# Optimization experiments

Measured on AMD Instinct MI355X. Metric: run time of the kernel, lower is better.

Reference implementation:

```python
import jax, jax.numpy as jnp
import numpy as np

H, DH = 8, 64            # heads, dim_head (inner_dim = 512)
W_DOT = 1.0              # mask_cond['para']['w_dot']
TOTAL_STEP = 50


def split_heads(x):
    # 'b n (h d) -> (b h) n d'
    b, n, _ = x.shape
    return x.reshape(b, n, H, DH).transpose(0, 2, 1, 3).reshape(b * H, n, DH)


def merge_heads(x):
    # '(b h) n d -> b n (h d)'
    bh, n, d = x.shape
    b = bh // H
    return x.reshape(b, H, n, d).transpose(0, 2, 1, 3).reshape(b, n, H * d)


def setup_inputs() -> dict:
    key = jax.random.key(0)
    ks = jax.random.split(key, 10)
    B, N, DQ, DC, L, C = 1, 4096, 320, 768, 77, 4
    INNER = H * DH
    w = lambda i, shape: jax.random.normal(ks[i], shape, jnp.float32) * 0.02
    return {
        "x": jax.random.normal(ks[0], (2 * B, N, DQ), jnp.float32),
        "uc_context": jax.random.normal(ks[1], (B, L, DC), jnp.float32),
        "ck": jax.random.normal(ks[2], (C, B, L, DC), jnp.float32),
        "cv": jax.random.normal(ks[3], (C, B, L, DC), jnp.float32),
        "attn_extra": jax.random.uniform(ks[4], (H, N, L), jnp.float32),
        "Wq": w(5, (DQ, INNER)),
        "Wk": w(6, (DC, INNER)),
        "Wv": w(7, (DC, INNER)),
        "Wo": w(8, (INNER, DQ)),
        "bo": jnp.zeros((DQ,), jnp.float32),
        "t": 10,
    }


def reference(x, uc_context, ck, cv, attn_extra, Wq, Wk, Wv, Wo, bo, t):
    scale = DH ** (-0.5)
    # schedule()['linear'][TOTAL_STEP - t - 1] == t / 50 * 4.6
    weight = (t / TOTAL_STEP) * 4.6

    B = uc_context.shape[0]
    true_bs = B * H

    q = split_heads(x @ Wq)                          # [(2B)H, N, d]
    k_uc = split_heads(uc_context @ Wk)              # [BH, L, d]
    v_uc = split_heads(uc_context @ Wv)
    k_c = jax.vmap(lambda c: split_heads(c @ Wk))(ck)  # [C, BH, L, d]
    v_c = jax.vmap(lambda c: split_heads(c @ Wv))(cv)

    q_uc, q_c = q[:true_bs], q[true_bs:]
    sim_uc = jnp.einsum('bid,bjd->bij', q_uc, k_uc) * scale     # [BH, N, L]
    sim_c = jnp.einsum('bid,cbjd->cbij', q_c, k_c) * scale      # [C, BH, N, L]

    # region-dependent additive soft mask on the first conditional branch,
    # weighted by w_dot * schedule_weight * max(sim_c[0])
    wmask = W_DOT * weight * sim_c[0].max()
    sim_c = sim_c.at[0].add(wmask * attn_extra)     # attn_extra [H, N, L] broadcasts (B=1)

    attn_uc = jax.nn.softmax(sim_uc, axis=-1)
    attn_c = jax.nn.softmax(sim_c, axis=-1)

    out_uc = jnp.einsum('bij,bjd->bid', attn_uc, v_uc)
    out_c = jnp.einsum('cbij,cbjd->bid', attn_c, v_c) / v_c.shape[0]

    out = jnp.concatenate([out_uc, out_c], axis=0)  # [2BH, N, d]
    out = merge_heads(out)                          # [2B, N, inner]
    return out @ Wo + bo                            # to_out (dropout=0 -> identity)
```

## Files before the change

### kernel.cpp

```cpp
#include <hip/hip_runtime.h>


typedef __attribute__((ext_vector_type(8))) short          bf16x8;
typedef __attribute__((ext_vector_type(4))) float          f32x4;
typedef __attribute__((ext_vector_type(8))) unsigned short u16x8;

#define OFF_XB    0ull
#define OFF_CTXB  5242880ull
#define OFF_WQT   6307328ull
#define OFF_WKT   6635008ull
#define OFF_WVT   7421440ull
#define OFF_WOT   8207872ull
#define OFF_QB    8535552ull
#define OFF_KB    16924160ull
#define OFF_VTB   17333760ull
#define OFF_ATT0  18152960ull
#define OFF_ATTC  22347264ull
#define OFF_MAX   39124480ull

#define SMEM_BYTES 38400

struct Params {
  const float *x, *uc, *ck, *cv, *ex, *Wq, *Wk, *Wv, *Wo, *bo;
  const int* tp;
  unsigned short *xb, *ctxb, *WqT, *WkT, *WvT, *WoT, *qb, *kb, *vtb, *att0, *attc;
  unsigned* maxslot;
  float* out;
};

__device__ __forceinline__ unsigned short bf_cvt(float f) {
  unsigned u = __float_as_uint(f);
  unsigned r = u + 0x7FFFu + ((u >> 16) & 1u);
  return (unsigned short)(r >> 16);
}
__device__ __forceinline__ float bf2f(unsigned short u) {
  return __uint_as_float(((unsigned)u) << 16);
}
__device__ __forceinline__ unsigned enc_f(float f) {
  int b = __float_as_int(f);
  return (b >= 0) ? ((unsigned)b | 0x80000000u) : ~(unsigned)b;
}
__device__ __forceinline__ float dec_f(unsigned u) {
  unsigned b = (u & 0x80000000u) ? (u ^ 0x80000000u) : ~u;
  return __int_as_float((int)b);
}
__device__ __forceinline__ f32x4 mfma16(bf16x8 a, bf16x8 b, f32x4 c) {
  return __builtin_amdgcn_mfma_f32_16x16x32_bf16(a, b, c, 0, 0, 0);
}
__device__ __forceinline__ void gload16(const void* g, void* l) {
  __builtin_amdgcn_global_load_lds((const __attribute__((address_space(1))) void*)g,
                                   (__attribute__((address_space(3))) void*)l, 16, 0, 0);
}

__global__ void __launch_bounds__(256, 4) k_all(Params p, int ph) {
  __shared__ __align__(16) char smem[SMEM_BYTES];
  const int tid  = threadIdx.x;
  const int lane = tid & 63, w = tid >> 6;
  const int l15  = lane & 15, qd = lane >> 4;
  const int v = blockIdx.x;

  if (ph == 0) {
    if (v < 2560) {
      size_t idx = (size_t)v * 256 + tid;
      float4 t = reinterpret_cast<const float4*>(p.x)[idx];
      ushort4 o = {bf_cvt(t.x), bf_cvt(t.y), bf_cvt(t.z), bf_cvt(t.w)};
      reinterpret_cast<ushort4*>(p.xb)[idx] = o;
      if (v == 0 && tid == 0) *p.maxslot = 0u;
    } else if (v < 3080) {
      size_t r = (size_t)(v - 2560) * 256 + tid;
      if (r < 133056) {
        const float4* s = (r < 14784) ? (reinterpret_cast<const float4*>(p.uc) + r)
                        : (r < 73920) ? (reinterpret_cast<const float4*>(p.ck) + (r - 14784))
                                      : (reinterpret_cast<const float4*>(p.cv) + (r - 73920));
        float4 t = *s;
        ushort4 o = {bf_cvt(t.x), bf_cvt(t.y), bf_cvt(t.z), bf_cvt(t.w)};
        reinterpret_cast<ushort4*>(p.ctxb)[r] = o;
      }
    } else {
      int q = v - 3080;
      const float* src; unsigned short* dst; int R, C, rt, ct;
      if (q < 160)      { src = p.Wq; dst = p.WqT; R = 320; C = 512; rt = q / 16; ct = q % 16; }
      else if (q < 544) { q -= 160; src = p.Wk; dst = p.WkT; R = 768; C = 512; rt = q / 16; ct = q % 16; }
      else if (q < 928) { q -= 544; src = p.Wv; dst = p.WvT; R = 768; C = 512; rt = q / 16; ct = q % 16; }
      else              { q -= 928; src = p.Wo; dst = p.WoT; R = 512; C = 320; rt = q / 10; ct = q % 10; }
      float* T = reinterpret_cast<float*>(smem);
      int r0 = rt * 32, c0 = ct * 32;
      { int r = tid >> 3, c4 = (tid & 7) * 4;
        float4 t = *reinterpret_cast<const float4*>(src + (size_t)(r0 + r) * C + c0 + c4);
        T[r * 33 + c4] = t.x; T[r * 33 + c4 + 1] = t.y;
        T[r * 33 + c4 + 2] = t.z; T[r * 33 + c4 + 3] = t.w; }
      __syncthreads();
      { int c = tid >> 3, r4 = (tid & 7) * 4;
        ushort4 o = {bf_cvt(T[r4 * 33 + c]), bf_cvt(T[(r4 + 1) * 33 + c]),
                     bf_cvt(T[(r4 + 2) * 33 + c]), bf_cvt(T[(r4 + 3) * 33 + c])};
        *reinterpret_cast<ushort4*>(dst + (size_t)(c0 + c) * R + r0 + r4) = o; }
    }
  }

  else if (ph == 1) {
    if (v < 512) {
      int mb = (v >> 3) * 128, nb = (v & 7) * 64;
      unsigned short* As = reinterpret_cast<unsigned short*>(smem);
      unsigned short* Bs = reinterpret_cast<unsigned short*>(smem + 8192);
      int wr = w >> 1, wc = w & 1;
      f32x4 acc[4][2] = {};
      for (int k0 = 0; k0 < 320; k0 += 32) {
#pragma unroll
        for (int ii = 0; ii < 2; ++ii) {
          int i = w * 2 + ii;
          int r = i * 16 + (lane >> 2), cs = lane & 3;
          gload16(p.xb + (size_t)(mb + r) * 320 + k0 + ((cs ^ (r & 3)) * 8), As + i * 512);
        }
        { int r = w * 16 + (lane >> 2), cs = lane & 3;
          gload16(p.WqT + (size_t)(nb + r) * 320 + k0 + ((cs ^ (r & 3)) * 8), Bs + w * 512); }
        __syncthreads();
        bf16x8 a[4], b[2];
#pragma unroll
        for (int mi = 0; mi < 4; ++mi) {
          int row = wr * 64 + mi * 16 + l15;
          a[mi] = *reinterpret_cast<const bf16x8*>(&As[row * 32 + ((qd ^ (row & 3)) * 8)]);
        }
#pragma unroll
        for (int ni = 0; ni < 2; ++ni) {
          int row = wc * 32 + ni * 16 + l15;
          b[ni] = *reinterpret_cast<const bf16x8*>(&Bs[row * 32 + ((qd ^ (row & 3)) * 8)]);
        }
#pragma unroll
        for (int mi = 0; mi < 4; ++mi)
#pragma unroll
          for (int ni = 0; ni < 2; ++ni)
            acc[mi][ni] = mfma16(a[mi], b[ni], acc[mi][ni]);
        __syncthreads();
      }
#pragma unroll
      for (int mi = 0; mi < 4; ++mi)
#pragma unroll
        for (int ni = 0; ni < 2; ++ni)
#pragma unroll
          for (int r = 0; r < 4; ++r) {
            int m = mb + wr * 64 + mi * 16 + qd * 4 + r;
            int n = nb + wc * 32 + ni * 16 + l15;
            int b_ = m >> 12, i = m & 4095, h = n >> 6, d = n & 63;
            p.qb[((size_t)((b_ * 8 + h) * 4096 + i)) * 64 + d] = bf_cvt(acc[mi][ni][r]);
          }
    } else {
      int u2 = v - 512;
      int g = u2 >> 3, nb = (u2 & 7) * 64;
      int kv = g >= 5, cidx = g % 5;
      int s77 = kv ? (cidx == 0 ? 0 : 4 + cidx) : (cidx == 0 ? 0 : cidx);
      const unsigned short* WT = kv ? p.WvT : p.WkT;
      unsigned short* Ac = reinterpret_cast<unsigned short*>(smem);
      unsigned short* Bc = reinterpret_cast<unsigned short*>(smem + 10240);
      f32x4 acc[5] = {};
      for (int k0 = 0; k0 < 768; k0 += 64) {
#pragma unroll
        for (int t = 0; t < 3; ++t) {
          int i = w + t * 4;
          if (i < 10) {
            int r = i * 8 + (lane >> 3), cs = lane & 7;
            gload16(p.ctxb + (size_t)(s77 * 77 + r) * 768 + k0 + ((cs ^ (r & 7)) * 8),
                    Ac + i * 512);
          }
        }
#pragma unroll
        for (int t = 0; t < 2; ++t) {
          int i = w * 2 + t;
          int r = i * 8 + (lane >> 3), cs = lane & 7;
          gload16(WT + (size_t)(nb + r) * 768 + k0 + ((cs ^ (r & 7)) * 8), Bc + i * 512);
        }
        __syncthreads();
#pragma unroll
        for (int ks = 0; ks < 2; ++ks) {
          int rb = w * 16 + l15;
          bf16x8 b = *reinterpret_cast<const bf16x8*>(&Bc[rb * 64 + (((ks * 4 + qd) ^ (rb & 7)) * 8)]);
#pragma unroll
          for (int mi = 0; mi < 5; ++mi) {
            int ra = mi * 16 + l15;
            bf16x8 a = *reinterpret_cast<const bf16x8*>(&Ac[ra * 64 + (((ks * 4 + qd) ^ (ra & 7)) * 8)]);
            acc[mi] = mfma16(a, b, acc[mi]);
          }
        }
        __syncthreads();
      }
#pragma unroll
      for (int mi = 0; mi < 5; ++mi)
#pragma unroll
        for (int r = 0; r < 4; ++r) {
          int j = mi * 16 + qd * 4 + r;
          int n = nb + w * 16 + l15, h = n >> 6, d = n & 63;
          unsigned short val = (j < 77) ? bf_cvt(acc[mi][r]) : (unsigned short)0;
          if (kv) p.vtb[((size_t)(cidx * 8 + h) * 64 + d) * 80 + j] = val;
          else    p.kb[((size_t)(cidx * 8 + h) * 80 + j) * 64 + d] = val;
        }
    }
  }

  else if (ph == 2) {
    int rt = v >> 3, h = v & 7;
    int rowbase = rt * 64;
    unsigned short* Ks = reinterpret_cast<unsigned short*>(smem);
    size_t kbase = (size_t)(1 * 8 + h) * 80 * 64;
    for (int u = tid; u < 640; u += 256) {
      int r = u >> 3, c8 = (u & 7) * 8;
      *reinterpret_cast<u16x8*>(&Ks[r * 72 + c8]) =
          *reinterpret_cast<const u16x8*>(&p.kb[kbase + (size_t)r * 64 + c8]);
    }
    __syncthreads();
    int myrow = rowbase + w * 16 + l15;
    bf16x8 aq0 = *reinterpret_cast<const bf16x8*>(&p.qb[((size_t)(8 + h) * 4096 + myrow) * 64 + qd * 8]);
    bf16x8 aq1 = *reinterpret_cast<const bf16x8*>(&p.qb[((size_t)(8 + h) * 4096 + myrow) * 64 + qd * 8 + 32]);
    float lmax = -3.4e38f;
#pragma unroll
    for (int jf = 0; jf < 5; ++jf) {
      bf16x8 b0 = *reinterpret_cast<const bf16x8*>(&Ks[(jf * 16 + l15) * 72 + qd * 8]);
      bf16x8 b1 = *reinterpret_cast<const bf16x8*>(&Ks[(jf * 16 + l15) * 72 + qd * 8 + 32]);
      f32x4 s = {};
      s = mfma16(aq0, b0, s);
      s = mfma16(aq1, b1, s);
      if (jf * 16 + l15 < 77) {
#pragma unroll
        for (int r = 0; r < 4; ++r) lmax = fmaxf(lmax, s[r] * 0.125f);
      }
    }
    for (int m = 1; m < 64; m <<= 1) lmax = fmaxf(lmax, __shfl_xor(lmax, m, 64));
    float* red = reinterpret_cast<float*>(smem + 11776);
    if (lane == 0) red[w] = lmax;
    __syncthreads();
    if (tid == 0)
      atomicMax(p.maxslot, enc_f(fmaxf(fmaxf(red[0], red[1]), fmaxf(red[2], red[3]))));
  }

  else if (ph == 3) {
    const float weight = ((float)(*p.tp)) * (4.6f / 50.0f);
    int rt = v / 40, rem = v % 40;
    int h = rem / 5, slot = rem % 5;
    int rowbase = rt * 64;
    int bh = slot ? 8 + h : h;
    unsigned short* Ks = reinterpret_cast<unsigned short*>(smem);
    unsigned short* VT = reinterpret_cast<unsigned short*>(smem + 11520);
    unsigned short* Ps = reinterpret_cast<unsigned short*>(smem + 24832);
    for (int u = tid; u < 1024; u += 256) {
      int d = u >> 4, j = 80 + (u & 15);
      VT[d * 104 + j] = 0; Ps[d * 104 + j] = 0;
    }
    size_t kbase = (size_t)(slot * 8 + h) * 80 * 64;
    size_t vbase = (size_t)(slot * 8 + h) * 64 * 80;
    for (int u = tid; u < 640; u += 256) {
      int r = u >> 3, c8 = (u & 7) * 8;
      *reinterpret_cast<u16x8*>(&Ks[r * 72 + c8]) =
          *reinterpret_cast<const u16x8*>(&p.kb[kbase + (size_t)r * 64 + c8]);
    }
    for (int u = tid; u < 640; u += 256) {
      int d = u / 10, c8 = (u % 10) * 8;
      *reinterpret_cast<u16x8*>(&VT[d * 104 + c8]) =
          *reinterpret_cast<const u16x8*>(&p.vtb[vbase + (size_t)d * 80 + c8]);
    }
    int myrow = rowbase + w * 16 + l15;
    bf16x8 aq0 = *reinterpret_cast<const bf16x8*>(&p.qb[((size_t)bh * 4096 + myrow) * 64 + qd * 8]);
    bf16x8 aq1 = *reinterpret_cast<const bf16x8*>(&p.qb[((size_t)bh * 4096 + myrow) * 64 + qd * 8 + 32]);
    __syncthreads();
    f32x4 sim[5];
#pragma unroll
    for (int jf = 0; jf < 5; ++jf) {
      bf16x8 b0 = *reinterpret_cast<const bf16x8*>(&Ks[(jf * 16 + l15) * 72 + qd * 8]);
      bf16x8 b1 = *reinterpret_cast<const bf16x8*>(&Ks[(jf * 16 + l15) * 72 + qd * 8 + 32]);
      f32x4 s = {};
      s = mfma16(aq0, b0, s);
      s = mfma16(aq1, b1, s);
      sim[jf] = s;
    }
    float wmask_ = (slot == 1) ? weight * dec_f(*p.maxslot) : 0.f;
    int grow = rowbase + w * 16 + qd * 4;
    float rowsum[4] = {0.f, 0.f, 0.f, 0.f};
    float e[5][4];
#pragma unroll
    for (int jf = 0; jf < 5; ++jf) {
      int j = jf * 16 + l15;
#pragma unroll
      for (int r = 0; r < 4; ++r) {
        float ev = 0.f;
        if (j < 77) {
          float val = sim[jf][r] * 0.125f;
          if (slot == 1) val += wmask_ * p.ex[((size_t)h * 4096 + grow + r) * 77 + j];
          ev = __expf(val);
        }
        e[jf][r] = ev;
        rowsum[r] += ev;
      }
    }
#pragma unroll
    for (int r = 0; r < 4; ++r) {
      float s = rowsum[r];
      s += __shfl_xor(s, 1, 64); s += __shfl_xor(s, 2, 64);
      s += __shfl_xor(s, 4, 64); s += __shfl_xor(s, 8, 64);
      rowsum[r] = 1.0f / s;
    }
#pragma unroll
    for (int jf = 0; jf < 5; ++jf) {
      int j = jf * 16 + l15;
#pragma unroll
      for (int r = 0; r < 4; ++r)
        Ps[(w * 16 + qd * 4 + r) * 104 + j] = bf_cvt(e[jf][r] * rowsum[r]);
    }
    bf16x8 pa[3];
#pragma unroll
    for (int ks = 0; ks < 3; ++ks)
      pa[ks] = *reinterpret_cast<const bf16x8*>(&Ps[(w * 16 + l15) * 104 + qd * 8 + ks * 32]);
#pragma unroll
    for (int nf = 0; nf < 4; ++nf) {
      f32x4 o = {};
#pragma unroll
      for (int ks = 0; ks < 3; ++ks) {
        bf16x8 bv = *reinterpret_cast<const bf16x8*>(&VT[(nf * 16 + l15) * 104 + qd * 8 + ks * 32]);
        o = mfma16(pa[ks], bv, o);
      }
      if (slot == 0) {
#pragma unroll
        for (int r = 0; r < 4; ++r)
          p.att0[((size_t)(grow + r)) * 512 + h * 64 + nf * 16 + l15] = bf_cvt(o[r]);
      } else {
#pragma unroll
        for (int r = 0; r < 4; ++r)
          p.attc[((size_t)((slot - 1) * 4096 + grow + r)) * 512 + h * 64 + nf * 16 + l15] = bf_cvt(o[r]);
      }
    }
  }

  else {
    int mb = (v / 5) * 64, nb = (v % 5) * 64;
    bool ucpart = (mb < 4096);
    int mb2 = mb - 4096;
    unsigned short* As = reinterpret_cast<unsigned short*>(smem);
    unsigned short* Bs = reinterpret_cast<unsigned short*>(smem + 5120);
    f32x4 acc[4] = {};
    for (int k0 = 0; k0 < 512; k0 += 32) {
      { int r = tid >> 2, cs = tid & 3;
        u16x8 val;
        if (ucpart) {
          val = *reinterpret_cast<const u16x8*>(&p.att0[(size_t)(mb + r) * 512 + k0 + cs * 8]);
        } else {
          float f[8] = {0.f, 0.f, 0.f, 0.f, 0.f, 0.f, 0.f, 0.f};
#pragma unroll
          for (int ci = 0; ci < 4; ++ci) {
            u16x8 t = *reinterpret_cast<const u16x8*>(
                &p.attc[((size_t)(ci * 4096 + mb2 + r)) * 512 + k0 + cs * 8]);
#pragma unroll
            for (int e2 = 0; e2 < 8; ++e2) f[e2] += bf2f((unsigned short)t[e2]);
          }
#pragma unroll
          for (int e2 = 0; e2 < 8; ++e2) val[e2] = bf_cvt(f[e2] * 0.25f);
        }
        *reinterpret_cast<u16x8*>(&As[r * 40 + cs * 8]) = val;
      }
      { int r = w * 16 + (lane >> 2), cs = lane & 3;
        gload16(p.WoT + (size_t)(nb + r) * 512 + k0 + ((cs ^ (r & 3)) * 8), Bs + w * 512); }
      __syncthreads();
      bf16x8 a = *reinterpret_cast<const bf16x8*>(&As[(w * 16 + l15) * 40 + qd * 8]);
#pragma unroll
      for (int nf = 0; nf < 4; ++nf) {
        int rb = nf * 16 + l15;
        bf16x8 b = *reinterpret_cast<const bf16x8*>(&Bs[rb * 32 + ((qd ^ (rb & 3)) * 8)]);
        acc[nf] = mfma16(a, b, acc[nf]);
      }
      __syncthreads();
    }
#pragma unroll
    for (int nf = 0; nf < 4; ++nf) {
      int n = nb + nf * 16 + l15;
      float bias = p.bo[n];
#pragma unroll
      for (int r = 0; r < 4; ++r)
        p.out[(size_t)(mb + w * 16 + qd * 4 + r) * 320 + n] = acc[nf][r] + bias;
    }
  }
}

extern "C" void kernel_launch(void* const* d_in, const int* in_sizes, int n_in,
                              void* d_out, int out_size, void* d_ws, size_t ws_size,
                              hipStream_t stream) {
  (void)in_sizes; (void)n_in; (void)out_size; (void)ws_size;
  char* base = (char*)d_ws;
  Params p;
  p.x  = (const float*)d_in[0];
  p.uc = (const float*)d_in[1];
  p.ck = (const float*)d_in[2];
  p.cv = (const float*)d_in[3];
  p.ex = (const float*)d_in[4];
  p.Wq = (const float*)d_in[5];
  p.Wk = (const float*)d_in[6];
  p.Wv = (const float*)d_in[7];
  p.Wo = (const float*)d_in[8];
  p.bo = (const float*)d_in[9];
  p.tp = (const int*)d_in[10];
  p.xb   = (unsigned short*)(base + OFF_XB);
  p.ctxb = (unsigned short*)(base + OFF_CTXB);
  p.WqT  = (unsigned short*)(base + OFF_WQT);
  p.WkT  = (unsigned short*)(base + OFF_WKT);
  p.WvT  = (unsigned short*)(base + OFF_WVT);
  p.WoT  = (unsigned short*)(base + OFF_WOT);
  p.qb   = (unsigned short*)(base + OFF_QB);
  p.kb   = (unsigned short*)(base + OFF_KB);
  p.vtb  = (unsigned short*)(base + OFF_VTB);
  p.att0 = (unsigned short*)(base + OFF_ATT0);
  p.attc = (unsigned short*)(base + OFF_ATTC);
  p.maxslot = (unsigned*)(base + OFF_MAX);
  p.out = (float*)d_out;

  k_all<<<4168, 256, 0, stream>>>(p, 0);
  k_all<<<592,  256, 0, stream>>>(p, 1);
  k_all<<<512,  256, 0, stream>>>(p, 2);
  k_all<<<2560, 256, 0, stream>>>(p, 3);
  k_all<<<640,  256, 0, stream>>>(p, 4);
}
```

Measured before the change: 158.4 us.

## Fuse bf16 conversions into GEMM loads and merge max reduction into Q projection

Removes the separate fp32-to-bf16 conversion passes for x and the contexts by converting inside the GEMM tile loads. The K/V projections now run in phase 0 alongside the weight transposes, reading fp32 Wk/Wv directly. The global max of the conditional scores is computed in the Q-projection epilogue, which eliminates a launch. The attention phase reads K and V straight from global memory instead of staging them in LDS, which cuts shared memory use and launches. The cost is redundant fp32 loads and conversions of weights per tile and uncached global reads inside attention.

Result: slower. 215.0 us (+35.7%).

```diff
diff --git a/kernel.cpp b/kernel.cpp
--- a/kernel.cpp
+++ b/kernel.cpp
@@ -5,25 +5,21 @@
 typedef __attribute__((ext_vector_type(4))) float          f32x4;
 typedef __attribute__((ext_vector_type(8))) unsigned short u16x8;
 
-#define OFF_XB    0ull
-#define OFF_CTXB  5242880ull
-#define OFF_WQT   6307328ull
-#define OFF_WKT   6635008ull
-#define OFF_WVT   7421440ull
-#define OFF_WOT   8207872ull
-#define OFF_QB    8535552ull
-#define OFF_KB    16924160ull
-#define OFF_VTB   17333760ull
-#define OFF_ATT0  18152960ull
-#define OFF_ATTC  22347264ull
-#define OFF_MAX   39124480ull
-
-#define SMEM_BYTES 38400
+#define OFF_WQT  0ull
+#define OFF_WOT  327680ull
+#define OFF_QB   655360ull
+#define OFF_KB   9043968ull
+#define OFF_VTB  9453568ull
+#define OFF_ATT0 10436608ull
+#define OFF_ATTC 14630912ull
+#define OFF_MAX  31408128ull
+
+#define SMEM_BYTES 22016
 
 struct Params {
   const float *x, *uc, *ck, *cv, *ex, *Wq, *Wk, *Wv, *Wo, *bo;
   const int* tp;
-  unsigned short *xb, *ctxb, *WqT, *WkT, *WvT, *WoT, *qb, *kb, *vtb, *att0, *attc;
+  unsigned short *WqT, *WoT, *qb, *kb, *vtb, *att0, *attc;
   unsigned* maxslot;
   float* out;
 };
@@ -53,37 +49,23 @@
 }
 
 __global__ void __launch_bounds__(256, 4) k_all(Params p, int ph) {
-  __shared__ __align__(16) char smem[SMEM_BYTES];
+  __shared__ __align__(16) char smem_raw[SMEM_BYTES];
+  unsigned short* smem = reinterpret_cast<unsigned short*>(smem_raw);
   const int tid  = threadIdx.x;
   const int lane = tid & 63, w = tid >> 6;
   const int l15  = lane & 15, qd = lane >> 4;
   const int v = blockIdx.x;
 
   if (ph == 0) {
-    if (v < 2560) {
-      size_t idx = (size_t)v * 256 + tid;
-      float4 t = reinterpret_cast<const float4*>(p.x)[idx];
-      ushort4 o = {bf_cvt(t.x), bf_cvt(t.y), bf_cvt(t.z), bf_cvt(t.w)};
-      reinterpret_cast<ushort4*>(p.xb)[idx] = o;
+    if (v < 320) {
       if (v == 0 && tid == 0) *p.maxslot = 0u;
-    } else if (v < 3080) {
-      size_t r = (size_t)(v - 2560) * 256 + tid;
-      if (r < 133056) {
-        const float4* s = (r < 14784) ? (reinterpret_cast<const float4*>(p.uc) + r)
-                        : (r < 73920) ? (reinterpret_cast<const float4*>(p.ck) + (r - 14784))
-                                      : (reinterpret_cast<const float4*>(p.cv) + (r - 73920));
-        float4 t = *s;
-        ushort4 o = {bf_cvt(t.x), bf_cvt(t.y), bf_cvt(t.z), bf_cvt(t.w)};
-        reinterpret_cast<ushort4*>(p.ctxb)[r] = o;
-      }
-    } else {
-      int q = v - 3080;
-      const float* src; unsigned short* dst; int R, C, rt, ct;
-      if (q < 160)      { src = p.Wq; dst = p.WqT; R = 320; C = 512; rt = q / 16; ct = q % 16; }
-      else if (q < 544) { q -= 160; src = p.Wk; dst = p.WkT; R = 768; C = 512; rt = q / 16; ct = q % 16; }
-      else if (q < 928) { q -= 544; src = p.Wv; dst = p.WvT; R = 768; C = 512; rt = q / 16; ct = q % 16; }
-      else              { q -= 928; src = p.Wo; dst = p.WoT; R = 512; C = 320; rt = q / 10; ct = q % 10; }
-      float* T = reinterpret_cast<float*>(smem);
+      int z = (v >= 160);
+      int q = z ? v - 160 : v;
+      const float* src = z ? p.Wo : p.Wq;
+      unsigned short* dst = z ? p.WoT : p.WqT;
+      int R = z ? 512 : 320, C = z ? 320 : 512;
+      int rt = z ? (q / 10) : (q / 16), ct = z ? (q % 10) : (q % 16);
+      float* T = reinterpret_cast<float*>(smem_raw);
       int r0 = rt * 32, c0 = ct * 32;
       { int r = tid >> 3, c4 = (tid & 7) * 4;
         float4 t = *reinterpret_cast<const float4*>(src + (size_t)(r0 + r) * C + c0 + c4);
@@ -94,89 +76,41 @@
         ushort4 o = {bf_cvt(T[r4 * 33 + c]), bf_cvt(T[(r4 + 1) * 33 + c]),
                      bf_cvt(T[(r4 + 2) * 33 + c]), bf_cvt(T[(r4 + 3) * 33 + c])};
         *reinterpret_cast<ushort4*>(dst + (size_t)(c0 + c) * R + r0 + r4) = o; }
-    }
-  }
-
-  else if (ph == 1) {
-    if (v < 512) {
-      int mb = (v >> 3) * 128, nb = (v & 7) * 64;
-      unsigned short* As = reinterpret_cast<unsigned short*>(smem);
-      unsigned short* Bs = reinterpret_cast<unsigned short*>(smem + 8192);
-      int wr = w >> 1, wc = w & 1;
-      f32x4 acc[4][2] = {};
-      for (int k0 = 0; k0 < 320; k0 += 32) {
-#pragma unroll
-        for (int ii = 0; ii < 2; ++ii) {
-          int i = w * 2 + ii;
-          int r = i * 16 + (lane >> 2), cs = lane & 3;
-          gload16(p.xb + (size_t)(mb + r) * 320 + k0 + ((cs ^ (r & 3)) * 8), As + i * 512);
-        }
-        { int r = w * 16 + (lane >> 2), cs = lane & 3;
-          gload16(p.WqT + (size_t)(nb + r) * 320 + k0 + ((cs ^ (r & 3)) * 8), Bs + w * 512); }
-        __syncthreads();
-        bf16x8 a[4], b[2];
-#pragma unroll
-        for (int mi = 0; mi < 4; ++mi) {
-          int row = wr * 64 + mi * 16 + l15;
-          a[mi] = *reinterpret_cast<const bf16x8*>(&As[row * 32 + ((qd ^ (row & 3)) * 8)]);
-        }
-#pragma unroll
-        for (int ni = 0; ni < 2; ++ni) {
-          int row = wc * 32 + ni * 16 + l15;
-          b[ni] = *reinterpret_cast<const bf16x8*>(&Bs[row * 32 + ((qd ^ (row & 3)) * 8)]);
-        }
-#pragma unroll
-        for (int mi = 0; mi < 4; ++mi)
-#pragma unroll
-          for (int ni = 0; ni < 2; ++ni)
-            acc[mi][ni] = mfma16(a[mi], b[ni], acc[mi][ni]);
-        __syncthreads();
-      }
-#pragma unroll
-      for (int mi = 0; mi < 4; ++mi)
-#pragma unroll
-        for (int ni = 0; ni < 2; ++ni)
-#pragma unroll
-          for (int r = 0; r < 4; ++r) {
-            int m = mb + wr * 64 + mi * 16 + qd * 4 + r;
-            int n = nb + wc * 32 + ni * 16 + l15;
-            int b_ = m >> 12, i = m & 4095, h = n >> 6, d = n & 63;
-            p.qb[((size_t)((b_ * 8 + h) * 4096 + i)) * 64 + d] = bf_cvt(acc[mi][ni][r]);
-          }
     } else {
-      int u2 = v - 512;
+      int u2 = v - 320;
       int g = u2 >> 3, nb = (u2 & 7) * 64;
       int kv = g >= 5, cidx = g % 5;
-      int s77 = kv ? (cidx == 0 ? 0 : 4 + cidx) : (cidx == 0 ? 0 : cidx);
-      const unsigned short* WT = kv ? p.WvT : p.WkT;
-      unsigned short* Ac = reinterpret_cast<unsigned short*>(smem);
-      unsigned short* Bc = reinterpret_cast<unsigned short*>(smem + 10240);
+      const float* csrc = (cidx == 0) ? p.uc
+                        : ((kv ? p.cv : p.ck) + (size_t)(cidx - 1) * 77 * 768);
+      const float* wsrc = kv ? p.Wv : p.Wk;
+      unsigned short* As = smem;
+      unsigned short* Bs = smem + 80 * 68;
       f32x4 acc[5] = {};
       for (int k0 = 0; k0 < 768; k0 += 64) {
-#pragma unroll
-        for (int t = 0; t < 3; ++t) {
-          int i = w + t * 4;
-          if (i < 10) {
-            int r = i * 8 + (lane >> 3), cs = lane & 7;
-            gload16(p.ctxb + (size_t)(s77 * 77 + r) * 768 + k0 + ((cs ^ (r & 7)) * 8),
-                    Ac + i * 512);
+        for (int u = tid; u < 1280; u += 256) {
+          int r = u >> 4, k4 = (u & 15) * 4;
+          ushort4 o = {0, 0, 0, 0};
+          if (r < 77) {
+            float4 t = *reinterpret_cast<const float4*>(csrc + (size_t)r * 768 + k0 + k4);
+            o.x = bf_cvt(t.x); o.y = bf_cvt(t.y); o.z = bf_cvt(t.z); o.w = bf_cvt(t.w);
           }
-        }
-#pragma unroll
-        for (int t = 0; t < 2; ++t) {
-          int i = w * 2 + t;
-          int r = i * 8 + (lane >> 3), cs = lane & 7;
-          gload16(WT + (size_t)(nb + r) * 768 + k0 + ((cs ^ (r & 7)) * 8), Bc + i * 512);
+          *reinterpret_cast<ushort4*>(&As[r * 68 + k4]) = o;
+        }
+        for (int u = tid; u < 1024; u += 256) {
+          int k = u >> 4, n4 = (u & 15) * 4;
+          float4 t = *reinterpret_cast<const float4*>(wsrc + (size_t)(k0 + k) * 512 + nb + n4);
+          Bs[(n4 + 0) * 72 + k] = bf_cvt(t.x);
+          Bs[(n4 + 1) * 72 + k] = bf_cvt(t.y);
+          Bs[(n4 + 2) * 72 + k] = bf_cvt(t.z);
+          Bs[(n4 + 3) * 72 + k] = bf_cvt(t.w);
         }
         __syncthreads();
 #pragma unroll
         for (int ks = 0; ks < 2; ++ks) {
-          int rb = w * 16 + l15;
-          bf16x8 b = *reinterpret_cast<const bf16x8*>(&Bc[rb * 64 + (((ks * 4 + qd) ^ (rb & 7)) * 8)]);
+          bf16x8 b = *reinterpret_cast<const bf16x8*>(&Bs[(w * 16 + l15) * 72 + qd * 8 + ks * 32]);
 #pragma unroll
           for (int mi = 0; mi < 5; ++mi) {
-            int ra = mi * 16 + l15;
-            bf16x8 a = *reinterpret_cast<const bf16x8*>(&Ac[ra * 64 + (((ks * 4 + qd) ^ (ra & 7)) * 8)]);
+            bf16x8 a = *reinterpret_cast<const bf16x8*>(&As[(mi * 16 + l15) * 68 + qd * 8 + ks * 32]);
             acc[mi] = mfma16(a, b, acc[mi]);
           }
         }
@@ -189,86 +123,133 @@
           int j = mi * 16 + qd * 4 + r;
           int n = nb + w * 16 + l15, h = n >> 6, d = n & 63;
           unsigned short val = (j < 77) ? bf_cvt(acc[mi][r]) : (unsigned short)0;
-          if (kv) p.vtb[((size_t)(cidx * 8 + h) * 64 + d) * 80 + j] = val;
-          else    p.kb[((size_t)(cidx * 8 + h) * 80 + j) * 64 + d] = val;
-        }
+          if (kv) p.vtb[((size_t)(cidx * 8 + h) * 64 + d) * 96 + j] = val;
+          else    p.kb [((size_t)(cidx * 8 + h) * 80 + j) * 64 + d] = val;
+        }
+      if (kv) {
+        for (int u = tid; u < 1024; u += 256) {
+          int dl = u >> 4, j = 80 + (u & 15);
+          int n = nb + dl, h = n >> 6, d = n & 63;
+          p.vtb[((size_t)(cidx * 8 + h) * 64 + d) * 96 + j] = 0;
+        }
+      }
     }
   }
 
+  else if (ph == 1) {
+    int mb = v >> 3, nb_i = v & 7;
+    int mb128 = mb * 128, nb = nb_i * 64;
+    unsigned short* As = smem;
+    unsigned short* Bs = smem + 128 * 40;
+    int wr = w >> 1, wc = w & 1;
+    f32x4 acc[4][2] = {};
+    for (int k0 = 0; k0 < 320; k0 += 32) {
+#pragma unroll
+      for (int i = 0; i < 4; ++i) {
+        int u = tid + i * 256;
+        int r = u >> 3, k4 = (u & 7) * 4;
+        float4 t = *reinterpret_cast<const float4*>(p.x + (size_t)(mb128 + r) * 320 + k0 + k4);
+        ushort4 o = {bf_cvt(t.x), bf_cvt(t.y), bf_cvt(t.z), bf_cvt(t.w)};
+        *reinterpret_cast<ushort4*>(&As[r * 40 + k4]) = o;
+      }
+      { int r = w * 16 + (lane >> 2), cs = lane & 3;
+        gload16(p.WqT + (size_t)(nb + r) * 320 + k0 + ((cs ^ (r & 3)) * 8), Bs + w * 512); }
+      __syncthreads();
+      bf16x8 a[4], b[2];
+#pragma unroll
+      for (int mi = 0; mi < 4; ++mi)
+        a[mi] = *reinterpret_cast<const bf16x8*>(&As[(wr * 64 + mi * 16 + l15) * 40 + qd * 8]);
+#pragma unroll
+      for (int ni = 0; ni < 2; ++ni) {
+        int row = wc * 32 + ni * 16 + l15;
+        b[ni] = *reinterpret_cast<const bf16x8*>(&Bs[row * 32 + ((qd ^ (row & 3)) * 8)]);
+      }
+#pragma unroll
+      for (int mi = 0; mi < 4; ++mi)
+#pragma unroll
+        for (int ni = 0; ni < 2; ++ni)
+          acc[mi][ni] = mfma16(a[mi], b[ni], acc[mi][ni]);
+      __syncthreads();
+    }
+#pragma unroll
+    for (int mi = 0; mi < 4; ++mi)
+#pragma unroll
+      for (int ni = 0; ni < 2; ++ni)
+#pragma unroll
+        for (int r = 0; r < 4; ++r) {
+          int m = mb128 + wr * 64 + mi * 16 + qd * 4 + r;
+          int d = wc * 32 + ni * 16 + l15;
+          int b_ = m >> 12, i = m & 4095;
+          p.qb[((size_t)((b_ * 8 + nb_i) * 4096 + i)) * 64 + d] = bf_cvt(acc[mi][ni][r]);
+        }
+    if (mb >= 32) {
+      unsigned short* Qt = smem;
+#pragma unroll
+      for (int mi = 0; mi < 4; ++mi)
+#pragma unroll
+        for (int ni = 0; ni < 2; ++ni)
+#pragma unroll
+          for (int r = 0; r < 4; ++r)
+            Qt[(wr * 64 + mi * 16 + qd * 4 + r) * 68 + wc * 32 + ni * 16 + l15] =
+                bf_cvt(acc[mi][ni][r]);
+      __syncthreads();
+      const unsigned short* kc = p.kb + (size_t)(1 * 8 + nb_i) * 80 * 64;
+      float lmax = -3.4e38f;
+#pragma unroll
+      for (int mg = 0; mg < 2; ++mg) {
+        int row = w * 32 + mg * 16 + l15;
+        bf16x8 a0 = *reinterpret_cast<const bf16x8*>(&Qt[row * 68 + qd * 8]);
+        bf16x8 a1 = *reinterpret_cast<const bf16x8*>(&Qt[row * 68 + qd * 8 + 32]);
+#pragma unroll
+        for (int jf = 0; jf < 5; ++jf) {
+          bf16x8 b0 = *reinterpret_cast<const bf16x8*>(&kc[(size_t)(jf * 16 + l15) * 64 + qd * 8]);
+          bf16x8 b1 = *reinterpret_cast<const bf16x8*>(&kc[(size_t)(jf * 16 + l15) * 64 + qd * 8 + 32]);
+          f32x4 s = {};
+          s = mfma16(a0, b0, s);
+          s = mfma16(a1, b1, s);
+          if (jf * 16 + l15 < 77) {
+#pragma unroll
+            for (int r = 0; r < 4; ++r) lmax = fmaxf(lmax, s[r]);
+          }
+        }
+      }
+      lmax *= 0.125f;
+      for (int m = 1; m < 64; m <<= 1) lmax = fmaxf(lmax, __shfl_xor(lmax, m, 64));
+      float* red = reinterpret_cast<float*>(smem_raw + 17408);
+      if (lane == 0) red[w] = lmax;
+      __syncthreads();
+      if (tid == 0)
+        atomicMax(p.maxslot, enc_f(fmaxf(fmaxf(red[0], red[1]), fmaxf(red[2], red[3]))));
+    }
+  }
+
   else if (ph == 2) {
-    int rt = v >> 3, h = v & 7;
-    int rowbase = rt * 64;
-    unsigned short* Ks = reinterpret_cast<unsigned short*>(smem);
-    size_t kbase = (size_t)(1 * 8 + h) * 80 * 64;
-    for (int u = tid; u < 640; u += 256) {
-      int r = u >> 3, c8 = (u & 7) * 8;
-      *reinterpret_cast<u16x8*>(&Ks[r * 72 + c8]) =
-          *reinterpret_cast<const u16x8*>(&p.kb[kbase + (size_t)r * 64 + c8]);
-    }
-    __syncthreads();
-    int myrow = rowbase + w * 16 + l15;
-    bf16x8 aq0 = *reinterpret_cast<const bf16x8*>(&p.qb[((size_t)(8 + h) * 4096 + myrow) * 64 + qd * 8]);
-    bf16x8 aq1 = *reinterpret_cast<const bf16x8*>(&p.qb[((size_t)(8 + h) * 4096 + myrow) * 64 + qd * 8 + 32]);
-    float lmax = -3.4e38f;
-#pragma unroll
-    for (int jf = 0; jf < 5; ++jf) {
-      bf16x8 b0 = *reinterpret_cast<const bf16x8*>(&Ks[(jf * 16 + l15) * 72 + qd * 8]);
-      bf16x8 b1 = *reinterpret_cast<const bf16x8*>(&Ks[(jf * 16 + l15) * 72 + qd * 8 + 32]);
-      f32x4 s = {};
-      s = mfma16(aq0, b0, s);
-      s = mfma16(aq1, b1, s);
-      if (jf * 16 + l15 < 77) {
-#pragma unroll
-        for (int r = 0; r < 4; ++r) lmax = fmaxf(lmax, s[r] * 0.125f);
-      }
-    }
-    for (int m = 1; m < 64; m <<= 1) lmax = fmaxf(lmax, __shfl_xor(lmax, m, 64));
-    float* red = reinterpret_cast<float*>(smem + 11776);
-    if (lane == 0) red[w] = lmax;
-    __syncthreads();
-    if (tid == 0)
-      atomicMax(p.maxslot, enc_f(fmaxf(fmaxf(red[0], red[1]), fmaxf(red[2], red[3]))));
-  }
-
-  else if (ph == 3) {
-    const float weight = ((float)(*p.tp)) * (4.6f / 50.0f);
     int rt = v / 40, rem = v % 40;
     int h = rem / 5, slot = rem % 5;
     int rowbase = rt * 64;
     int bh = slot ? 8 + h : h;
-    unsigned short* Ks = reinterpret_cast<unsigned short*>(smem);
-    unsigned short* VT = reinterpret_cast<unsigned short*>(smem + 11520);
-    unsigned short* Ps = reinterpret_cast<unsigned short*>(smem + 24832);
+    unsigned short* Ps = smem;
     for (int u = tid; u < 1024; u += 256) {
       int d = u >> 4, j = 80 + (u & 15);
-      VT[d * 104 + j] = 0; Ps[d * 104 + j] = 0;
-    }
-    size_t kbase = (size_t)(slot * 8 + h) * 80 * 64;
-    size_t vbase = (size_t)(slot * 8 + h) * 64 * 80;
-    for (int u = tid; u < 640; u += 256) {
-      int r = u >> 3, c8 = (u & 7) * 8;
-      *reinterpret_cast<u16x8*>(&Ks[r * 72 + c8]) =
-          *reinterpret_cast<const u16x8*>(&p.kb[kbase + (size_t)r * 64 + c8]);
-    }
-    for (int u = tid; u < 640; u += 256) {
-      int d = u / 10, c8 = (u % 10) * 8;
-      *reinterpret_cast<u16x8*>(&VT[d * 104 + c8]) =
-          *reinterpret_cast<const u16x8*>(&p.vtb[vbase + (size_t)d * 80 + c8]);
-    }
+      Ps[d * 104 + j] = 0;
+    }
+    __syncthreads();
+    const unsigned short* kc = p.kb + (size_t)(slot * 8 + h) * 80 * 64;
+    const unsigned short* vc = p.vtb + (size_t)(slot * 8 + h) * 64 * 96;
     int myrow = rowbase + w * 16 + l15;
     bf16x8 aq0 = *reinterpret_cast<const bf16x8*>(&p.qb[((size_t)bh * 4096 + myrow) * 64 + qd * 8]);
     bf16x8 aq1 = *reinterpret_cast<const bf16x8*>(&p.qb[((size_t)bh * 4096 + myrow) * 64 + qd * 8 + 32]);
-    __syncthreads();
     f32x4 sim[5];
 #pragma unroll
     for (int jf = 0; jf < 5; ++jf) {
-      bf16x8 b0 = *reinterpret_cast<const bf16x8*>(&Ks[(jf * 16 + l15) * 72 + qd * 8]);
-      bf16x8 b1 = *reinterpret_cast<const bf16x8*>(&Ks[(jf * 16 + l15) * 72 + qd * 8 + 32]);
+      bf16x8 b0 = *reinterpret_cast<const bf16x8*>(&kc[(size_t)(jf * 16 + l15) * 64 + qd * 8]);
+      bf16x8 b1 = *reinterpret_cast<const bf16x8*>(&kc[(size_t)(jf * 16 + l15) * 64 + qd * 8 + 32]);
       f32x4 s = {};
       s = mfma16(aq0, b0, s);
       s = mfma16(aq1, b1, s);
       sim[jf] = s;
     }
+    const float weight = ((float)(*p.tp)) * (4.6f / 50.0f);
     float wmask_ = (slot == 1) ? weight * dec_f(*p.maxslot) : 0.f;
     int grow = rowbase + w * 16 + qd * 4;
     float rowsum[4] = {0.f, 0.f, 0.f, 0.f};
@@ -311,7 +292,7 @@
       f32x4 o = {};
 #pragma unroll
       for (int ks = 0; ks < 3; ++ks) {
-        bf16x8 bv = *reinterpret_cast<const bf16x8*>(&VT[(nf * 16 + l15) * 104 + qd * 8 + ks * 32]);
+        bf16x8 bv = *reinterpret_cast<const bf16x8*>(&vc[(size_t)(nf * 16 + l15) * 96 + qd * 8 + ks * 32]);
         o = mfma16(pa[ks], bv, o);
       }
       if (slot == 0) {
@@ -330,8 +311,8 @@
     int mb = (v / 5) * 64, nb = (v % 5) * 64;
     bool ucpart = (mb < 4096);
     int mb2 = mb - 4096;
-    unsigned short* As = reinterpret_cast<unsigned short*>(smem);
-    unsigned short* Bs = reinterpret_cast<unsigned short*>(smem + 5120);
+    unsigned short* As = smem;
+    unsigned short* Bs = smem + 64 * 40;
     f32x4 acc[4] = {};
     for (int k0 = 0; k0 < 512; k0 += 32) {
       { int r = tid >> 2, cs = tid & 3;
@@ -392,11 +373,7 @@
   p.Wo = (const float*)d_in[8];
   p.bo = (const float*)d_in[9];
   p.tp = (const int*)d_in[10];
-  p.xb   = (unsigned short*)(base + OFF_XB);
-  p.ctxb = (unsigned short*)(base + OFF_CTXB);
   p.WqT  = (unsigned short*)(base + OFF_WQT);
-  p.WkT  = (unsigned short*)(base + OFF_WKT);
-  p.WvT  = (unsigned short*)(base + OFF_WVT);
   p.WoT  = (unsigned short*)(base + OFF_WOT);
   p.qb   = (unsigned short*)(base + OFF_QB);
   p.kb   = (unsigned short*)(base + OFF_KB);
@@ -406,9 +383,8 @@
   p.maxslot = (unsigned*)(base + OFF_MAX);
   p.out = (float*)d_out;
 
-  k_all<<<4168, 256, 0, stream>>>(p, 0);
-  k_all<<<592,  256, 0, stream>>>(p, 1);
-  k_all<<<512,  256, 0, stream>>>(p, 2);
-  k_all<<<2560, 256, 0, stream>>>(p, 3);
-  k_all<<<640,  256, 0, stream>>>(p, 4);
-}
+  k_all<<<400,  256, 0, stream>>>(p, 0);
+  k_all<<<512,  256, 0, stream>>>(p, 1);
+  k_all<<<2560, 256, 0, stream>>>(p, 2);
+  k_all<<<640,  256, 0, stream>>>(p, 3);
+}
```
